# Kernel optimization log

Hardware: AMD Instinct MI355X
Metric: run time of the kernel (lower is better)

## Reference

```python
import jax, jax.numpy as jnp
import numpy as np

TOP_K = 8  # num_experts_per_tok
NEG_INF = -1e9


def setup_inputs() -> dict:
    key = jax.random.key(0)
    ks = jax.random.split(key, 6)
    B, S, H, I, E, G, GS = 1, 2048, 2048, 1408, 64, 8, 8
    sc = 0.02
    return {
        "hidden_states": jax.random.normal(ks[0], (B, S, H), jnp.float32),
        "gate_w": jax.random.normal(ks[1], (E, H), jnp.float32) * sc,
        "mask_up_w": jax.random.normal(ks[2], (G, H, GS), jnp.float32) * sc,
        "gate_proj_w": jax.random.normal(ks[3], (G, I, H), jnp.float32) * sc,
        "up_proj_w": jax.random.normal(ks[4], (G, I, H), jnp.float32) * sc,
        "down_proj_w": jax.random.normal(ks[5], (G, H, I), jnp.float32) * sc,
        "inv_map": jnp.arange(G * GS, dtype=jnp.int64).reshape(G, GS),
    }


def reference(hidden_states, gate_w, mask_up_w, gate_proj_w, up_proj_w, down_proj_w, inv_map):
    B, S, H = hidden_states.shape
    x = hidden_states.reshape(-1, H)  # [N, H]
    N = x.shape[0]
    E = gate_w.shape[0]

    # Gate: softmax scores -> top-k routing (DeepSeek-style MoEGate)
    scores = jax.nn.softmax(x @ gate_w.T, axis=-1)          # [N, E]
    topk_w, topk_idx = jax.lax.top_k(scores, TOP_K)         # [N, K]

    # Per-expert routing weight: w_e[t, e] = sum_k topk_w[t,k] * (topk_idx[t,k]==e)
    w_e = jnp.zeros((N, E), x.dtype).at[jnp.arange(N)[:, None], topk_idx].add(topk_w)

    # Gather group-local weights: flat[t, g, i] for sub-expert i of group g
    flat = w_e[:, inv_map]                                   # [N, G, GS]
    scalar = flat.sum(-1)                                    # [N, G]
    soft = jax.nn.softmax(jnp.where(flat == 0, NEG_INF, flat), axis=-1)  # [N, G, GS]

    # Mask injection: x' = x + mask_up_proj(soft)
    xg = x[:, None, :] + jnp.einsum('ngi,ghi->ngh', soft, mask_up_w)     # [N, G, H]

    # SwiGLU per group
    g = jnp.einsum('ngh,gih->ngi', xg, gate_proj_w)          # [N, G, I]
    u = jnp.einsum('ngh,gih->ngi', xg, up_proj_w)            # [N, G, I]
    a = jax.nn.silu(g) * u
    d = jnp.einsum('ngi,ghi->ngh', a, down_proj_w)           # [N, G, H]

    # scalar * output, accumulated over groups (scalar==0 rows contribute 0,
    # matching the original's zero-masked scatter)
    y = jnp.einsum('ng,ngh->nh', scalar, d)
    return y.reshape(B, S, H)
```

## Files before the change

kernel.cpp:

```cpp
#include <hip/hip_runtime.h>

#define N_TOK 2048
#define H_DIM 2048
#define I_DIM 1408
#define E_EXP 64
#define G_GRP 8
#define KTOT  (G_GRP * I_DIM)
#define NQ    (G_GRP * I_DIM * H_DIM / 4)
#define NQB   (NQ / 256)

typedef __bf16 bf16x8 __attribute__((ext_vector_type(8)));
typedef float f32x4 __attribute__((ext_vector_type(4)));

__device__ __forceinline__ unsigned short f2bf(float f) {
    unsigned int u = __builtin_bit_cast(unsigned int, f);
    u += 0x7fffu + ((u >> 16) & 1u);
    return (unsigned short)(u >> 16);
}

__device__ __forceinline__ void gl_lds16(const void* g, void* l) {
    __builtin_amdgcn_global_load_lds(
        (const __attribute__((address_space(1))) unsigned int*)g,
        (__attribute__((address_space(3))) unsigned int*)l, 16, 0, 0);
}

__device__ __forceinline__ bf16x8 lds_frag(const unsigned short* sm, int row, int c) {
    return *(const bf16x8*)&sm[(row * 8 + (c ^ (row & 7))) * 8];
}

__global__ __launch_bounds__(256) void k_prep(const float* __restrict__ gw,
                                              const float* __restrict__ wgp,
                                              const float* __restrict__ wup,
                                              const float* __restrict__ wdp,
                                              float* __restrict__ gwT,
                                              unsigned short* __restrict__ wgB,
                                              unsigned short* __restrict__ wuB,
                                              unsigned short* __restrict__ wdB) {
    int b = blockIdx.x, t = threadIdx.x;
    if (b < 2 * NQB) {
        const float* in = (b < NQB) ? wgp : wup;
        unsigned short* out = (b < NQB) ? wgB : wuB;
        int i = (b < NQB ? b : b - NQB) * 256 + t;
        float4 v = ((const float4*)in)[i];
        ushort4 o;
        o.x = f2bf(v.x); o.y = f2bf(v.y); o.z = f2bf(v.z); o.w = f2bf(v.w);
        ((ushort4*)out)[i] = o;
    } else if (b < 3 * NQB) {
        int idx = (b - 2 * NQB) * 256 + t;
        int i4 = idx % (I_DIM / 4);
        int h  = (idx / (I_DIM / 4)) & (H_DIM - 1);
        int g  = idx / ((I_DIM / 4) * H_DIM);
        float4 v = ((const float4*)(wdp + ((size_t)g * H_DIM + h) * I_DIM))[i4];
        ushort4 o;
        o.x = f2bf(v.x); o.y = f2bf(v.y); o.z = f2bf(v.z); o.w = f2bf(v.w);
        ((ushort4*)(wdB + ((size_t)h * G_GRP + g) * I_DIM))[i4] = o;
    } else {
        int i = (b - 3 * NQB) * 256 + t;
        gwT[i] = gw[(i & 63) * H_DIM + (i >> 6)];
    }
}

__global__ __launch_bounds__(512) void k_gating(const float* __restrict__ x,
                                                const float* __restrict__ gwT,
                                                float* __restrict__ soft,
                                                float* __restrict__ scal) {
    __shared__ double smAcc[8][8][64];
    int t = threadIdx.x, wid = t >> 6, lane = t & 63;
    int n0 = blockIdx.x * 8;

    double acc[8];
#pragma unroll
    for (int k = 0; k < 8; ++k) acc[k] = 0.0;
    int h0 = wid * 256;
    for (int h = h0; h < h0 + 256; ++h) {
        float gv = gwT[h * 64 + lane];
#pragma unroll
        for (int tok = 0; tok < 8; ++tok)
            acc[tok] += (double)x[(size_t)(n0 + tok) * H_DIM + h] * (double)gv;
    }
#pragma unroll
    for (int tok = 0; tok < 8; ++tok) smAcc[wid][tok][lane] = acc[tok];
    __syncthreads();

    double lg = 0.0;
#pragma unroll
    for (int w2 = 0; w2 < 8; ++w2) lg += smAcc[w2][wid][lane];
    float logit = (float)lg;

    float mx = logit;
#pragma unroll
    for (int d = 1; d < 64; d <<= 1) mx = fmaxf(mx, __shfl_xor(mx, d));
    float ex = expf(logit - mx);
    float sm = ex;
#pragma unroll
    for (int d = 1; d < 64; d <<= 1) sm += __shfl_xor(sm, d);
    float prob = ex / sm;

    float cur = prob, w = 0.0f;
#pragma unroll
    for (int it = 0; it < 8; ++it) {
        float m = cur;
#pragma unroll
        for (int d = 1; d < 64; d <<= 1) m = fmaxf(m, __shfl_xor(m, d));
        unsigned long long msk = __ballot(cur == m);
        int first = __ffsll(msk) - 1;
        if (lane == first) { w = prob; cur = -1.0f; }
    }
    float wf = w;

    float s8 = wf;
#pragma unroll
    for (int d = 1; d < 8; d <<= 1) s8 += __shfl_xor(s8, d);
    float v = (wf == 0.0f) ? -1000000000.0f : wf;
    float m8 = v;
#pragma unroll
    for (int d = 1; d < 8; d <<= 1) m8 = fmaxf(m8, __shfl_xor(m8, d));
    float e8 = expf(v - m8);
    float q8 = e8;
#pragma unroll
    for (int d = 1; d < 8; d <<= 1) q8 += __shfl_xor(q8, d);

    int n = n0 + wid;
    soft[(size_t)n * 64 + lane] = e8 / q8;
    if ((lane & 7) == 0) scal[(size_t)n * 8 + (lane >> 3)] = s8;
}

__global__ __launch_bounds__(256) void k_xg(const float* __restrict__ x,
                                            const float* __restrict__ muw,
                                            const float* __restrict__ soft,
                                            unsigned short* __restrict__ xg) {
    int g = blockIdx.z, h0 = blockIdx.y * 1024, n0 = blockIdx.x * 128;
    __shared__ float smSf[128][8];
    int t = threadIdx.x;
    {
        int r = t >> 1, s4 = (t & 1) * 4;
        float4 sv = *(const float4*)&soft[(size_t)(n0 + r) * 64 + g * 8 + s4];
        smSf[r][s4 + 0] = sv.x; smSf[r][s4 + 1] = sv.y;
        smSf[r][s4 + 2] = sv.z; smSf[r][s4 + 3] = sv.w;
    }
    int hh = t * 4;
    float mu[8][4];
#pragma unroll
    for (int j = 0; j < 4; ++j) {
        const float4* p = (const float4*)(muw + ((size_t)g * H_DIM + h0 + hh + j) * 8);
        float4 a = p[0], b = p[1];
        mu[0][j] = a.x; mu[1][j] = a.y; mu[2][j] = a.z; mu[3][j] = a.w;
        mu[4][j] = b.x; mu[5][j] = b.y; mu[6][j] = b.z; mu[7][j] = b.w;
    }
    __syncthreads();
    for (int r = 0; r < 128; ++r) {
        float4 xv = *(const float4*)&x[(size_t)(n0 + r) * H_DIM + h0 + hh];
        float c0 = xv.x, c1 = xv.y, c2 = xv.z, c3 = xv.w;
#pragma unroll
        for (int s = 0; s < 8; ++s) {
            float w = smSf[r][s];
            c0 += w * mu[s][0]; c1 += w * mu[s][1];
            c2 += w * mu[s][2]; c3 += w * mu[s][3];
        }
        ushort4 o;
        o.x = f2bf(c0); o.y = f2bf(c1); o.z = f2bf(c2); o.w = f2bf(c3);
        *(ushort4*)&xg[((size_t)g * N_TOK + n0 + r) * H_DIM + h0 + hh] = o;
    }
}

__global__ __launch_bounds__(256) void k_gemm1(const unsigned short* __restrict__ xg,
                                               const unsigned short* __restrict__ wg,
                                               const unsigned short* __restrict__ wu,
                                               const float* __restrict__ scal,
                                               unsigned short* __restrict__ aB) {
    int f = blockIdx.x;
    int g = f & 7, r = f >> 3;
    int m0 = (r & 15) * 128;
    int n0 = (r >> 4) * 64;
    __shared__ __align__(16) unsigned short smA[8192];
    __shared__ __align__(16) unsigned short smG[4096];
    __shared__ __align__(16) unsigned short smU[4096];
    __shared__ float smS[128];
    int t = threadIdx.x, wid = t >> 6, lane = t & 63;
    int r16 = lane & 15, quad = lane >> 4;
    int wm = wid >> 1, wn = wid & 1;

    if (t < 128) smS[t] = scal[(size_t)(m0 + t) * 8 + g];

    const unsigned short* A  = xg + (size_t)g * N_TOK * H_DIM;
    const unsigned short* Bg = wg + (size_t)g * I_DIM * H_DIM;
    const unsigned short* Bu = wu + (size_t)g * I_DIM * H_DIM;

    f32x4 zero = {0.f, 0.f, 0.f, 0.f};
    f32x4 accg[4][2], accu[4][2];
#pragma unroll
    for (int mi = 0; mi < 4; ++mi)
#pragma unroll
        for (int ni = 0; ni < 2; ++ni) { accg[mi][ni] = zero; accu[mi][ni] = zero; }

    for (int k0 = 0; k0 < H_DIM; k0 += 64) {
#pragma unroll
        for (int j = 0; j < 4; ++j) {
            int issue = wid * 4 + j;
            int s = issue * 64 + lane;
            int row = s >> 3;
            int c = (s & 7) ^ (row & 7);
            gl_lds16(A + (size_t)(m0 + row) * H_DIM + k0 + c * 8, &smA[issue * 512]);
        }
#pragma unroll
        for (int j = 0; j < 2; ++j) {
            int issue = wid * 2 + j;
            int s = issue * 64 + lane;
            int row = s >> 3;
            int c = (s & 7) ^ (row & 7);
            gl_lds16(Bg + (size_t)(n0 + row) * H_DIM + k0 + c * 8, &smG[issue * 512]);
            gl_lds16(Bu + (size_t)(n0 + row) * H_DIM + k0 + c * 8, &smU[issue * 512]);
        }
        __syncthreads();
#pragma unroll
        for (int kh = 0; kh < 2; ++kh) {
            int cc = kh * 4 + quad;
            bf16x8 af[4], bgf[2], buf_[2];
#pragma unroll
            for (int mi = 0; mi < 4; ++mi) af[mi] = lds_frag(smA, wm * 64 + mi * 16 + r16, cc);
#pragma unroll
            for (int ni = 0; ni < 2; ++ni) {
                int rw = wn * 32 + ni * 16 + r16;
                bgf[ni] = lds_frag(smG, rw, cc);
                buf_[ni] = lds_frag(smU, rw, cc);
            }
#pragma unroll
            for (int mi = 0; mi < 4; ++mi)
#pragma unroll
                for (int ni = 0; ni < 2; ++ni) {
                    accg[mi][ni] = __builtin_amdgcn_mfma_f32_16x16x32_bf16(af[mi], bgf[ni], accg[mi][ni], 0, 0, 0);
                    accu[mi][ni] = __builtin_amdgcn_mfma_f32_16x16x32_bf16(af[mi], buf_[ni], accu[mi][ni], 0, 0, 0);
                }
        }
        __syncthreads();
    }

#pragma unroll
    for (int mi = 0; mi < 4; ++mi)
#pragma unroll
        for (int ni = 0; ni < 2; ++ni)
#pragma unroll
            for (int rr = 0; rr < 4; ++rr) {
                int rl = wm * 64 + mi * 16 + quad * 4 + rr;
                int row = m0 + rl;
                int col = n0 + wn * 32 + ni * 16 + r16;
                float gv = accg[mi][ni][rr];
                float sv = gv / (1.0f + __expf(-gv));
                aB[((size_t)row * G_GRP + g) * I_DIM + col] = f2bf(sv * accu[mi][ni][rr] * smS[rl]);
            }
}

__global__ __launch_bounds__(256) void k_gemm2(const unsigned short* __restrict__ aB,
                                               const unsigned short* __restrict__ wd,
                                               float* __restrict__ out) {
    int m0 = blockIdx.x * 128, h0 = blockIdx.y * 128;
    int kbase = blockIdx.z * (KTOT / 2);
    __shared__ __align__(16) unsigned short smA[8192], smB[8192];
    int t = threadIdx.x, wid = t >> 6, lane = t & 63;
    int r16 = lane & 15, quad = lane >> 4;
    int wm = wid >> 1, wn = wid & 1;

    f32x4 zero = {0.f, 0.f, 0.f, 0.f};
    f32x4 acc[4][4];
#pragma unroll
    for (int mi = 0; mi < 4; ++mi)
#pragma unroll
        for (int ni = 0; ni < 4; ++ni) acc[mi][ni] = zero;

    for (int k0 = kbase; k0 < kbase + KTOT / 2; k0 += 64) {
#pragma unroll
        for (int j = 0; j < 4; ++j) {
            int issue = wid * 4 + j;
            int s = issue * 64 + lane;
            int row = s >> 3;
            int c = (s & 7) ^ (row & 7);
            gl_lds16(aB + (size_t)(m0 + row) * KTOT + k0 + c * 8, &smA[issue * 512]);
            gl_lds16(wd + (size_t)(h0 + row) * KTOT + k0 + c * 8, &smB[issue * 512]);
        }
        __syncthreads();
#pragma unroll
        for (int kh = 0; kh < 2; ++kh) {
            int cc = kh * 4 + quad;
            bf16x8 af[4], bf_[4];
#pragma unroll
            for (int mi = 0; mi < 4; ++mi) af[mi]  = lds_frag(smA, wm * 64 + mi * 16 + r16, cc);
#pragma unroll
            for (int ni = 0; ni < 4; ++ni) bf_[ni] = lds_frag(smB, wn * 64 + ni * 16 + r16, cc);
#pragma unroll
            for (int mi = 0; mi < 4; ++mi)
#pragma unroll
                for (int ni = 0; ni < 4; ++ni)
                    acc[mi][ni] = __builtin_amdgcn_mfma_f32_16x16x32_bf16(af[mi], bf_[ni], acc[mi][ni], 0, 0, 0);
        }
        __syncthreads();
    }

#pragma unroll
    for (int mi = 0; mi < 4; ++mi)
#pragma unroll
        for (int ni = 0; ni < 4; ++ni)
#pragma unroll
            for (int rr = 0; rr < 4; ++rr) {
                int row = m0 + wm * 64 + mi * 16 + quad * 4 + rr;
                int col = h0 + wn * 64 + ni * 16 + r16;
                atomicAdd(&out[(size_t)row * H_DIM + col], acc[mi][ni][rr]);
            }
}

extern "C" void kernel_launch(void* const* d_in, const int* in_sizes, int n_in,
                              void* d_out, int out_size, void* d_ws, size_t ws_size,
                              hipStream_t stream) {
    const float* x   = (const float*)d_in[0];
    const float* gw  = (const float*)d_in[1];
    const float* mu  = (const float*)d_in[2];
    const float* wgp = (const float*)d_in[3];
    const float* wup = (const float*)d_in[4];
    const float* wdp = (const float*)d_in[5];
    float* out = (float*)d_out;
    char* ws = (char*)d_ws;

    float* gwT  = (float*)(ws + 0);
    float* soft = (float*)(ws + 524288);
    float* scal = (float*)(ws + 1048576);
    unsigned short* wgB = (unsigned short*)(ws + 1114112);
    unsigned short* wuB = (unsigned short*)(ws + 47251456);
    unsigned short* wdB = (unsigned short*)(ws + 93388800);
    unsigned short* xg  = (unsigned short*)(ws + 139526144);
    unsigned short* aB  = (unsigned short*)(ws + 206635008);

    hipMemsetAsync(d_out, 0, (size_t)N_TOK * H_DIM * sizeof(float), stream);
    k_prep<<<3 * NQB + 512, 256, 0, stream>>>(gw, wgp, wup, wdp, gwT, wgB, wuB, wdB);
    k_gating<<<N_TOK / 8, 512, 0, stream>>>(x, gwT, soft, scal);
    k_xg<<<dim3(16, 2, 8), 256, 0, stream>>>(x, mu, soft, xg);
    k_gemm1<<<2816, 256, 0, stream>>>(xg, wgB, wuB, scal, aB);
    k_gemm2<<<dim3(16, 16, 2), 256, 0, stream>>>(aB, wdB, out);
}
```

Before: 824.6 us.

## Double-buffer LDS tiles with BK=32 in both GEMMs and split-K 4 in gemm2

Both GEMM kernels now use two LDS buffers of K-depth 32 (instead of a single buffer of 64), so the next tile's global-to-LDS loads are issued before computing the current tile. This leaves one barrier per iteration instead of two. gemm2 also raises split-K from 2 to 4 for more blocks, at the cost of more atomic adds to the output. The smaller K tile means more loop iterations and barriers per unit of work.

New measurement: 831.8 us. Within noise of the previous version (+0.9%).

```diff
diff --git a/kernel.cpp b/kernel.cpp
--- a/kernel.cpp
+++ b/kernel.cpp
@@ -24,8 +24,8 @@
         (__attribute__((address_space(3))) unsigned int*)l, 16, 0, 0);
 }
 
-__device__ __forceinline__ bf16x8 lds_frag(const unsigned short* sm, int row, int c) {
-    return *(const bf16x8*)&sm[(row * 8 + (c ^ (row & 7))) * 8];
+__device__ __forceinline__ bf16x8 frag32(const unsigned short* sm, int row, int cc) {
+    return *(const bf16x8*)&sm[(row * 4 + (cc ^ (row & 3))) * 8];
 }
 
 __global__ __launch_bounds__(256) void k_prep(const float* __restrict__ gw,
@@ -172,9 +172,9 @@
     int g = f & 7, r = f >> 3;
     int m0 = (r & 15) * 128;
     int n0 = (r >> 4) * 64;
-    __shared__ __align__(16) unsigned short smA[8192];
-    __shared__ __align__(16) unsigned short smG[4096];
-    __shared__ __align__(16) unsigned short smU[4096];
+    __shared__ __align__(16) unsigned short smA0[4096], smA1[4096];
+    __shared__ __align__(16) unsigned short smG0[2048], smG1[2048];
+    __shared__ __align__(16) unsigned short smU0[2048], smU1[2048];
     __shared__ float smS[128];
     int t = threadIdx.x, wid = t >> 6, lane = t & 63;
     int r16 = lane & 15, quad = lane >> 4;
@@ -186,6 +186,27 @@
     const unsigned short* Bg = wg + (size_t)g * I_DIM * H_DIM;
     const unsigned short* Bu = wu + (size_t)g * I_DIM * H_DIM;
 
+    int sA0 = (wid * 2 + 0) * 64 + lane, sA1 = (wid * 2 + 1) * 64 + lane;
+    int rA0 = sA0 >> 2, rA1 = sA1 >> 2;
+    int cA0 = (sA0 & 3) ^ (rA0 & 3), cA1 = (sA1 & 3) ^ (rA1 & 3);
+    const unsigned short* pA0 = A + (size_t)(m0 + rA0) * H_DIM + cA0 * 8;
+    const unsigned short* pA1 = A + (size_t)(m0 + rA1) * H_DIM + cA1 * 8;
+    int sB = wid * 64 + lane;
+    int rB = sB >> 2, cB = (sB & 3) ^ (rB & 3);
+    const unsigned short* pG = Bg + (size_t)(n0 + rB) * H_DIM + cB * 8;
+    const unsigned short* pU = Bu + (size_t)(n0 + rB) * H_DIM + cB * 8;
+
+    unsigned short *aCur = smA0, *aNxt = smA1;
+    unsigned short *gCur = smG0, *gNxt = smG1;
+    unsigned short *uCur = smU0, *uNxt = smU1;
+    int dA0 = (wid * 2 + 0) * 512, dA1 = (wid * 2 + 1) * 512, dB = wid * 512;
+
+    gl_lds16(pA0, aCur + dA0);
+    gl_lds16(pA1, aCur + dA1);
+    gl_lds16(pG,  gCur + dB);
+    gl_lds16(pU,  uCur + dB);
+    pA0 += 32; pA1 += 32; pG += 32; pU += 32;
+
     f32x4 zero = {0.f, 0.f, 0.f, 0.f};
     f32x4 accg[4][2], accu[4][2];
 #pragma unroll
@@ -193,46 +214,37 @@
 #pragma unroll
         for (int ni = 0; ni < 2; ++ni) { accg[mi][ni] = zero; accu[mi][ni] = zero; }
 
-    for (int k0 = 0; k0 < H_DIM; k0 += 64) {
-#pragma unroll
-        for (int j = 0; j < 4; ++j) {
-            int issue = wid * 4 + j;
-            int s = issue * 64 + lane;
-            int row = s >> 3;
-            int c = (s & 7) ^ (row & 7);
-            gl_lds16(A + (size_t)(m0 + row) * H_DIM + k0 + c * 8, &smA[issue * 512]);
+    __syncthreads();
+
+    for (int it = 0; it < H_DIM / 32; ++it) {
+        if (it + 1 < H_DIM / 32) {
+            gl_lds16(pA0, aNxt + dA0);
+            gl_lds16(pA1, aNxt + dA1);
+            gl_lds16(pG,  gNxt + dB);
+            gl_lds16(pU,  uNxt + dB);
+            pA0 += 32; pA1 += 32; pG += 32; pU += 32;
         }
-#pragma unroll
-        for (int j = 0; j < 2; ++j) {
-            int issue = wid * 2 + j;
-            int s = issue * 64 + lane;
-            int row = s >> 3;
-            int c = (s & 7) ^ (row & 7);
-            gl_lds16(Bg + (size_t)(n0 + row) * H_DIM + k0 + c * 8, &smG[issue * 512]);
-            gl_lds16(Bu + (size_t)(n0 + row) * H_DIM + k0 + c * 8, &smU[issue * 512]);
+        bf16x8 af[4], bgf[2], buf_[2];
+#pragma unroll
+        for (int mi = 0; mi < 4; ++mi) af[mi] = frag32(aCur, wm * 64 + mi * 16 + r16, quad);
+#pragma unroll
+        for (int ni = 0; ni < 2; ++ni) {
+            int rw = wn * 32 + ni * 16 + r16;
+            bgf[ni] = frag32(gCur, rw, quad);
+            buf_[ni] = frag32(uCur, rw, quad);
         }
+#pragma unroll
+        for (int mi = 0; mi < 4; ++mi)
+#pragma unroll
+            for (int ni = 0; ni < 2; ++ni) {
+                accg[mi][ni] = __builtin_amdgcn_mfma_f32_16x16x32_bf16(af[mi], bgf[ni], accg[mi][ni], 0, 0, 0);
+                accu[mi][ni] = __builtin_amdgcn_mfma_f32_16x16x32_bf16(af[mi], buf_[ni], accu[mi][ni], 0, 0, 0);
+            }
         __syncthreads();
-#pragma unroll
-        for (int kh = 0; kh < 2; ++kh) {
-            int cc = kh * 4 + quad;
-            bf16x8 af[4], bgf[2], buf_[2];
-#pragma unroll
-            for (int mi = 0; mi < 4; ++mi) af[mi] = lds_frag(smA, wm * 64 + mi * 16 + r16, cc);
-#pragma unroll
-            for (int ni = 0; ni < 2; ++ni) {
-                int rw = wn * 32 + ni * 16 + r16;
-                bgf[ni] = lds_frag(smG, rw, cc);
-                buf_[ni] = lds_frag(smU, rw, cc);
-            }
-#pragma unroll
-            for (int mi = 0; mi < 4; ++mi)
-#pragma unroll
-                for (int ni = 0; ni < 2; ++ni) {
-                    accg[mi][ni] = __builtin_amdgcn_mfma_f32_16x16x32_bf16(af[mi], bgf[ni], accg[mi][ni], 0, 0, 0);
-                    accu[mi][ni] = __builtin_amdgcn_mfma_f32_16x16x32_bf16(af[mi], buf_[ni], accu[mi][ni], 0, 0, 0);
-                }
-        }
-        __syncthreads();
+        unsigned short* tp;
+        tp = aCur; aCur = aNxt; aNxt = tp;
+        tp = gCur; gCur = gNxt; gNxt = tp;
+        tp = uCur; uCur = uNxt; uNxt = tp;
     }
 
 #pragma unroll
@@ -254,12 +266,31 @@
                                                const unsigned short* __restrict__ wd,
                                                float* __restrict__ out) {
     int m0 = blockIdx.x * 128, h0 = blockIdx.y * 128;
-    int kbase = blockIdx.z * (KTOT / 2);
-    __shared__ __align__(16) unsigned short smA[8192], smB[8192];
+    int kbase = blockIdx.z * (KTOT / 4);
+    __shared__ __align__(16) unsigned short smA0[4096], smA1[4096];
+    __shared__ __align__(16) unsigned short smB0[4096], smB1[4096];
     int t = threadIdx.x, wid = t >> 6, lane = t & 63;
     int r16 = lane & 15, quad = lane >> 4;
     int wm = wid >> 1, wn = wid & 1;
 
+    int s0 = (wid * 2 + 0) * 64 + lane, s1 = (wid * 2 + 1) * 64 + lane;
+    int r0 = s0 >> 2, r1 = s1 >> 2;
+    int c0 = (s0 & 3) ^ (r0 & 3), c1 = (s1 & 3) ^ (r1 & 3);
+    const unsigned short* pA0 = aB + (size_t)(m0 + r0) * KTOT + kbase + c0 * 8;
+    const unsigned short* pA1 = aB + (size_t)(m0 + r1) * KTOT + kbase + c1 * 8;
+    const unsigned short* pB0 = wd + (size_t)(h0 + r0) * KTOT + kbase + c0 * 8;
+    const unsigned short* pB1 = wd + (size_t)(h0 + r1) * KTOT + kbase + c1 * 8;
+
+    unsigned short *aCur = smA0, *aNxt = smA1;
+    unsigned short *bCur = smB0, *bNxt = smB1;
+    int d0 = (wid * 2 + 0) * 512, d1 = (wid * 2 + 1) * 512;
+
+    gl_lds16(pA0, aCur + d0);
+    gl_lds16(pA1, aCur + d1);
+    gl_lds16(pB0, bCur + d0);
+    gl_lds16(pB1, bCur + d1);
+    pA0 += 32; pA1 += 32; pB0 += 32; pB1 += 32;
+
     f32x4 zero = {0.f, 0.f, 0.f, 0.f};
     f32x4 acc[4][4];
 #pragma unroll
@@ -267,32 +298,30 @@
 #pragma unroll
         for (int ni = 0; ni < 4; ++ni) acc[mi][ni] = zero;
 
-    for (int k0 = kbase; k0 < kbase + KTOT / 2; k0 += 64) {
-#pragma unroll
-        for (int j = 0; j < 4; ++j) {
-            int issue = wid * 4 + j;
-            int s = issue * 64 + lane;
-            int row = s >> 3;
-            int c = (s & 7) ^ (row & 7);
-            gl_lds16(aB + (size_t)(m0 + row) * KTOT + k0 + c * 8, &smA[issue * 512]);
-            gl_lds16(wd + (size_t)(h0 + row) * KTOT + k0 + c * 8, &smB[issue * 512]);
+    __syncthreads();
+
+    for (int it = 0; it < (KTOT / 4) / 32; ++it) {
+        if (it + 1 < (KTOT / 4) / 32) {
+            gl_lds16(pA0, aNxt + d0);
+            gl_lds16(pA1, aNxt + d1);
+            gl_lds16(pB0, bNxt + d0);
+            gl_lds16(pB1, bNxt + d1);
+            pA0 += 32; pA1 += 32; pB0 += 32; pB1 += 32;
         }
+        bf16x8 af[4], bf_[4];
+#pragma unroll
+        for (int mi = 0; mi < 4; ++mi) af[mi]  = frag32(aCur, wm * 64 + mi * 16 + r16, quad);
+#pragma unroll
+        for (int ni = 0; ni < 4; ++ni) bf_[ni] = frag32(bCur, wn * 64 + ni * 16 + r16, quad);
+#pragma unroll
+        for (int mi = 0; mi < 4; ++mi)
+#pragma unroll
+            for (int ni = 0; ni < 4; ++ni)
+                acc[mi][ni] = __builtin_amdgcn_mfma_f32_16x16x32_bf16(af[mi], bf_[ni], acc[mi][ni], 0, 0, 0);
         __syncthreads();
-#pragma unroll
-        for (int kh = 0; kh < 2; ++kh) {
-            int cc = kh * 4 + quad;
-            bf16x8 af[4], bf_[4];
-#pragma unroll
-            for (int mi = 0; mi < 4; ++mi) af[mi]  = lds_frag(smA, wm * 64 + mi * 16 + r16, cc);
-#pragma unroll
-            for (int ni = 0; ni < 4; ++ni) bf_[ni] = lds_frag(smB, wn * 64 + ni * 16 + r16, cc);
-#pragma unroll
-            for (int mi = 0; mi < 4; ++mi)
-#pragma unroll
-                for (int ni = 0; ni < 4; ++ni)
-                    acc[mi][ni] = __builtin_amdgcn_mfma_f32_16x16x32_bf16(af[mi], bf_[ni], acc[mi][ni], 0, 0, 0);
-        }
-        __syncthreads();
+        unsigned short* tp;
+        tp = aCur; aCur = aNxt; aNxt = tp;
+        tp = bCur; bCur = bNxt; bNxt = tp;
     }
 
 #pragma unroll
@@ -333,5 +362,5 @@
     k_gating<<<N_TOK / 8, 512, 0, stream>>>(x, gwT, soft, scal);
     k_xg<<<dim3(16, 2, 8), 256, 0, stream>>>(x, mu, soft, xg);
     k_gemm1<<<2816, 256, 0, stream>>>(xg, wgB, wuB, scal, aB);
-    k_gemm2<<<dim3(16, 16, 2), 256, 0, stream>>>(aB, wdB, out);
-}
+    k_gemm2<<<dim3(16, 16, 4), 256, 0, stream>>>(aB, wdB, out);
+}
```
